# Kernel optimization log

Measured on AMD Instinct MI355X. Metric: run time of the kernel, lower is better.

The kernel has to match this reference:

```python
import jax, jax.numpy as jnp
import numpy as np

N = 100000   # nodes
E = 1600000  # edges (avg degree 16)
D = 128      # in_channels
C = 40       # out_channels (classes)
K = 3        # propagation hops


def setup_inputs() -> dict:
    key = jax.random.key(0)
    k1, k2, k3 = jax.random.split(key, 3)
    x = jax.random.normal(k1, (N, D), dtype=jnp.float32)
    edge_index = jax.random.randint(k2, (2, E), 0, N, dtype=jnp.int64)
    W = jax.random.normal(k3, (D, C), dtype=jnp.float32) * (1.0 / np.sqrt(D))
    b = jnp.zeros((C,), dtype=jnp.float32)
    return {"x": x, "edge_index": edge_index, "W": W, "b": b}


def reference(x, edge_index, W, b):
    n = x.shape[0]
    # gcn_norm: add self-loops, symmetric degree normalization
    loop = jnp.arange(n, dtype=edge_index.dtype)
    src = jnp.concatenate([edge_index[0], loop])  # [E+N]
    dst = jnp.concatenate([edge_index[1], loop])  # [E+N]
    deg = jax.ops.segment_sum(jnp.ones(src.shape[0], x.dtype), dst, num_segments=n)
    deg_inv_sqrt = jnp.where(deg > 0, jax.lax.rsqrt(deg), 0.0)
    norm = deg_inv_sqrt[src] * deg_inv_sqrt[dst]  # [E+N]
    for _ in range(K):
        x = jax.ops.segment_sum(x[src] * norm[:, None], dst, num_segments=n)
    logits = x @ W + b  # [N, C]
    return jax.nn.log_softmax(logits, axis=1)
```

## Files before the change

### kernel.cpp

```cpp
#include <hip/hip_runtime.h>

#define D 128
#define C 40
#define NBH 256
#define BSH 8
#define NBKT_MAX 512
#define EPB 6272
#define ZS 16

typedef __attribute__((ext_vector_type(8))) short s8v;
typedef __attribute__((ext_vector_type(4))) float f4v;

__device__ __forceinline__ float bf2f(unsigned short u) {
    union { unsigned int i; float f; } v; v.i = ((unsigned int)u) << 16; return v.f;
}
__device__ __forceinline__ unsigned short f2bf(float f) {
    unsigned int x = __float_as_uint(f);
    unsigned int r = (x + 0x7FFFu + ((x >> 16) & 1u)) >> 16;
    return (unsigned short)r;
}

__global__ void hist_proj_kernel(const int* __restrict__ dst, int* __restrict__ M, int E,
                                 const float* __restrict__ x, const float* __restrict__ W,
                                 unsigned short* __restrict__ y, int n, int nbkt) {
    __shared__ int shist[NBKT_MAX];
    int bid = blockIdx.x, tid = threadIdx.x;
    int role, sub;
    if (bid < 2 * NBH) { role = bid & 1; sub = bid >> 1; }
    else { role = 0; sub = bid - NBH; }

    if (role == 1) {
        for (int t = tid; t < nbkt; t += 256) shist[t] = 0;
        __syncthreads();
        int chunk = (E + NBH - 1) / NBH;
        int base = sub * chunk;
        int lim = min(E, base + chunk);
        for (int e = base + tid; e < lim; e += 256)
            atomicAdd(&shist[dst[e] >> BSH], 1);
        __syncthreads();
        for (int t = tid; t < nbkt; t += 256) M[t * NBH + sub] = shist[t];
        return;
    }

    int wid = tid >> 6;
    int lane = tid & 63;
    int tile = sub * 4 + wid;
    if (tile * 16 >= n) return;
    int r = lane & 15;
    int kg = lane >> 4;

    s8v bfrag[3][4];
#pragma unroll
    for (int ct = 0; ct < 3; ++ct) {
        int col = ct * 16 + r;
#pragma unroll
        for (int ks = 0; ks < 4; ++ks) {
            s8v f;
#pragma unroll
            for (int j = 0; j < 8; ++j) {
                int k = ks * 32 + kg * 8 + j;
                float wv = (col < C) ? W[k * C + col] : 0.0f;
                f[j] = (short)f2bf(wv);
            }
            bfrag[ct][ks] = f;
        }
    }

    f4v acc0 = {0.f, 0.f, 0.f, 0.f};
    f4v acc1 = {0.f, 0.f, 0.f, 0.f};
    f4v acc2 = {0.f, 0.f, 0.f, 0.f};
    int row = tile * 16 + r;
    const float4* xrow = (const float4*)(x + (size_t)row * D);
#pragma unroll
    for (int ks = 0; ks < 4; ++ks) {
        int kb = ks * 32 + kg * 8;
        float4 u0 = xrow[kb >> 2];
        float4 u1 = xrow[(kb >> 2) + 1];
        s8v af;
        af[0] = (short)f2bf(u0.x); af[1] = (short)f2bf(u0.y);
        af[2] = (short)f2bf(u0.z); af[3] = (short)f2bf(u0.w);
        af[4] = (short)f2bf(u1.x); af[5] = (short)f2bf(u1.y);
        af[6] = (short)f2bf(u1.z); af[7] = (short)f2bf(u1.w);
        acc0 = __builtin_amdgcn_mfma_f32_16x16x32_bf16(af, bfrag[0][ks], acc0, 0, 0, 0);
        acc1 = __builtin_amdgcn_mfma_f32_16x16x32_bf16(af, bfrag[1][ks], acc1, 0, 0, 0);
        acc2 = __builtin_amdgcn_mfma_f32_16x16x32_bf16(af, bfrag[2][ks], acc2, 0, 0, 0);
    }
#pragma unroll
    for (int rg = 0; rg < 4; ++rg) {
        int orow = tile * 16 + kg * 4 + rg;
        unsigned short* yr = y + (size_t)orow * (ZS * 4);
        yr[r] = f2bf(acc0[rg]);
        yr[16 + r] = f2bf(acc1[rg]);
        if (r < 8) yr[32 + r] = f2bf(acc2[rg]);
    }
}

__global__ void scanM_kernel(int* __restrict__ M, int* __restrict__ btot, int nbkt) {
    __shared__ int s[NBH];
    int b = blockIdx.x, tid = threadIdx.x;
    int v = M[b * NBH + tid];
    s[tid] = v;
    __syncthreads();
    for (int off = 1; off < NBH; off <<= 1) {
        int t = (tid >= off) ? s[tid - off] : 0;
        __syncthreads();
        s[tid] += t;
        __syncthreads();
    }
    M[b * NBH + tid] = s[tid] - v;
    if (tid == NBH - 1) btot[b] = s[tid];
}

__global__ void scanB_kernel(const int* __restrict__ btot, int* __restrict__ bbase,
                             int* __restrict__ rowptr, int nbkt, int n, int E) {
    __shared__ int s[512];
    int tid = threadIdx.x;
    int v = (tid < nbkt) ? btot[tid] : 0;
    s[tid] = v;
    __syncthreads();
    for (int off = 1; off < 512; off <<= 1) {
        int t = (tid >= off) ? s[tid - off] : 0;
        __syncthreads();
        s[tid] += t;
        __syncthreads();
    }
    if (tid < nbkt) bbase[tid] = s[tid] - v;
    if (tid == 0) { bbase[nbkt] = E; rowptr[n] = E; }
}

__global__ void __launch_bounds__(256)
part_kernel(const int* __restrict__ src, const int* __restrict__ dst,
            const int* __restrict__ M, const int* __restrict__ bbase,
            int* __restrict__ ebuf, int E, int nbkt) {
    __shared__ int lhist[NBKT_MAX];
    __shared__ int ls[NBKT_MAX];
    __shared__ int lslot[NBKT_MAX];
    __shared__ int sdelta[NBKT_MAX];
    __shared__ int sVal[EPB];
    __shared__ int sG[EPB];
    int blk = blockIdx.x, tid = threadIdx.x;
    int chunk = (E + NBH - 1) / NBH;
    int base = blk * chunk;
    int lim = min(E, base + chunk);
    int cnt = lim - base;

    for (int t = tid; t < NBKT_MAX; t += 256) lhist[t] = 0;
    __syncthreads();
    for (int e = base + tid; e < lim; e += 256)
        atomicAdd(&lhist[dst[e] >> BSH], 1);
    __syncthreads();
    {
        int i0 = tid, i1 = tid + 256;
        ls[i0] = lhist[i0]; ls[i1] = lhist[i1];
        __syncthreads();
        for (int off = 1; off < 512; off <<= 1) {
            int v0 = (i0 >= off) ? ls[i0 - off] : 0;
            int v1 = (i1 >= off) ? ls[i1 - off] : 0;
            __syncthreads();
            ls[i0] += v0; ls[i1] += v1;
            __syncthreads();
        }
    }
    for (int t = tid; t < nbkt; t += 256) {
        int excl = ls[t] - lhist[t];
        lslot[t] = excl;
        sdelta[t] = bbase[t] + M[t * NBH + blk] - excl;
    }
    __syncthreads();
    for (int e = base + tid; e < lim; e += 256) {
        int d = dst[e];
        int t = d >> BSH;
        int slot = atomicAdd(&lslot[t], 1);
        sVal[slot] = src[e] | ((d & ((1 << BSH) - 1)) << 17);
        sG[slot] = sdelta[t] + slot;
    }
    __syncthreads();
    for (int i = tid; i < cnt; i += 256) ebuf[sG[i]] = sVal[i];
}

__global__ void bucket_csr_kernel(const int* __restrict__ ebuf, const int* __restrict__ bbase,
                                  int* __restrict__ rowptr, float* __restrict__ dis,
                                  int* __restrict__ srcs, unsigned short* __restrict__ y, int n) {
    __shared__ int scnt[256];
    __shared__ int s[256];
    __shared__ int sptr[256];
    __shared__ float sdis[256];
    int b = blockIdx.x, tid = threadIdx.x;
    int lo = bbase[b], hi = bbase[b + 1];
    scnt[tid] = 0;
    __syncthreads();
    for (int i = lo + tid; i < hi; i += 256)
        atomicAdd(&scnt[(ebuf[i] >> 17) & 255], 1);
    __syncthreads();
    int v = scnt[tid];
    s[tid] = v;
    __syncthreads();
    for (int off = 1; off < 256; off <<= 1) {
        int t = (tid >= off) ? s[tid - off] : 0;
        __syncthreads();
        s[tid] += t;
        __syncthreads();
    }
    int excl = s[tid] - v;
    int node = b * 256 + tid;
    float dv = rsqrtf(1.0f + (float)v);
    if (node < n) { rowptr[node] = lo + excl; dis[node] = dv; }
    sdis[tid] = dv;
    sptr[tid] = lo + excl;
    __syncthreads();
    for (int i = lo + tid; i < hi; i += 256) {
        int ev = ebuf[i];
        int pos = atomicAdd(&sptr[(ev >> 17) & 255], 1);
        srcs[pos] = ev & 0x1FFFF;
    }
    __syncthreads();
    ushort4* y4 = (ushort4*)y;
    size_t base4 = (size_t)b * 256 * ZS;
    for (int idx = tid; idx < 256 * ZS; idx += 256) {
        int ch = idx & (ZS - 1);
        int node2 = b * 256 + (idx >> 4);
        if (ch < 10 && node2 < n) {
            ushort4 u = y4[base4 + idx];
            float sc = sdis[idx >> 4];
            u.x = f2bf(sc * bf2f(u.x)); u.y = f2bf(sc * bf2f(u.y));
            u.z = f2bf(sc * bf2f(u.z)); u.w = f2bf(sc * bf2f(u.w));
            y4[base4 + idx] = u;
        }
    }
}

#define ACC(vv) { ax += bf2f(vv.x); ay += bf2f(vv.y); az += bf2f(vv.z); aw += bf2f(vv.w); }

__global__ void gatherZ_kernel(const unsigned short* __restrict__ zin,
                               unsigned short* __restrict__ zout,
                               const int* __restrict__ rowptr, const int* __restrict__ srcs,
                               const float* __restrict__ dis, int n) {
    int gtid = blockIdx.x * blockDim.x + threadIdx.x;
    int node = gtid / 10;
    int ch = gtid - node * 10;
    if (node >= n) return;
    const ushort4* zi = (const ushort4*)zin;
    ushort4 sv = zi[(size_t)node * ZS + ch];
    float ax = bf2f(sv.x), ay = bf2f(sv.y), az = bf2f(sv.z), aw = bf2f(sv.w);
    int beg = rowptr[node], end = rowptr[node + 1];
    int e = beg;
    for (; e + 8 <= end; e += 8) {
        int s0 = srcs[e + 0], s1 = srcs[e + 1], s2 = srcs[e + 2], s3 = srcs[e + 3];
        int s4 = srcs[e + 4], s5 = srcs[e + 5], s6 = srcs[e + 6], s7 = srcs[e + 7];
        ushort4 v0 = zi[(size_t)s0 * ZS + ch];
        ushort4 v1 = zi[(size_t)s1 * ZS + ch];
        ushort4 v2 = zi[(size_t)s2 * ZS + ch];
        ushort4 v3 = zi[(size_t)s3 * ZS + ch];
        ushort4 v4 = zi[(size_t)s4 * ZS + ch];
        ushort4 v5 = zi[(size_t)s5 * ZS + ch];
        ushort4 v6 = zi[(size_t)s6 * ZS + ch];
        ushort4 v7 = zi[(size_t)s7 * ZS + ch];
        ACC(v0) ACC(v1) ACC(v2) ACC(v3) ACC(v4) ACC(v5) ACC(v6) ACC(v7)
    }
    for (; e + 4 <= end; e += 4) {
        int s0 = srcs[e + 0], s1 = srcs[e + 1], s2 = srcs[e + 2], s3 = srcs[e + 3];
        ushort4 v0 = zi[(size_t)s0 * ZS + ch];
        ushort4 v1 = zi[(size_t)s1 * ZS + ch];
        ushort4 v2 = zi[(size_t)s2 * ZS + ch];
        ushort4 v3 = zi[(size_t)s3 * ZS + ch];
        ACC(v0) ACC(v1) ACC(v2) ACC(v3)
    }
    for (; e < end; ++e) {
        ushort4 vv = zi[(size_t)srcs[e] * ZS + ch];
        ACC(vv)
    }
    float dd = dis[node];
    float sc = dd * dd;
    ushort4 o;
    o.x = f2bf(ax * sc); o.y = f2bf(ay * sc); o.z = f2bf(az * sc); o.w = f2bf(aw * sc);
    ((ushort4*)zout)[(size_t)node * ZS + ch] = o;
}

__global__ void __launch_bounds__(320)
gatherZ_lsm_kernel(const unsigned short* __restrict__ zin, const float* __restrict__ b,
                   float* __restrict__ out, const int* __restrict__ rowptr,
                   const int* __restrict__ srcs, const float* __restrict__ dis, int n) {
    __shared__ float sY[32 * C];
    __shared__ float sb[C];
    int tid = threadIdx.x;
    if (tid < C) sb[tid] = b[tid];
    int ndb = tid / 10;
    int ch = tid - ndb * 10;
    int node = blockIdx.x * 32 + ndb;
    if (node < n) {
        const ushort4* zi = (const ushort4*)zin;
        ushort4 sv = zi[(size_t)node * ZS + ch];
        float ax = bf2f(sv.x), ay = bf2f(sv.y), az = bf2f(sv.z), aw = bf2f(sv.w);
        int beg = rowptr[node], end = rowptr[node + 1];
        int e = beg;
        for (; e + 8 <= end; e += 8) {
            int s0 = srcs[e + 0], s1 = srcs[e + 1], s2 = srcs[e + 2], s3 = srcs[e + 3];
            int s4 = srcs[e + 4], s5 = srcs[e + 5], s6 = srcs[e + 6], s7 = srcs[e + 7];
            ushort4 v0 = zi[(size_t)s0 * ZS + ch];
            ushort4 v1 = zi[(size_t)s1 * ZS + ch];
            ushort4 v2 = zi[(size_t)s2 * ZS + ch];
            ushort4 v3 = zi[(size_t)s3 * ZS + ch];
            ushort4 v4 = zi[(size_t)s4 * ZS + ch];
            ushort4 v5 = zi[(size_t)s5 * ZS + ch];
            ushort4 v6 = zi[(size_t)s6 * ZS + ch];
            ushort4 v7 = zi[(size_t)s7 * ZS + ch];
            ACC(v0) ACC(v1) ACC(v2) ACC(v3) ACC(v4) ACC(v5) ACC(v6) ACC(v7)
        }
        for (; e + 4 <= end; e += 4) {
            int s0 = srcs[e + 0], s1 = srcs[e + 1], s2 = srcs[e + 2], s3 = srcs[e + 3];
            ushort4 v0 = zi[(size_t)s0 * ZS + ch];
            ushort4 v1 = zi[(size_t)s1 * ZS + ch];
            ushort4 v2 = zi[(size_t)s2 * ZS + ch];
            ushort4 v3 = zi[(size_t)s3 * ZS + ch];
            ACC(v0) ACC(v1) ACC(v2) ACC(v3)
        }
        for (; e < end; ++e) {
            ushort4 vv = zi[(size_t)srcs[e] * ZS + ch];
            ACC(vv)
        }
        float dd = dis[node];
        ((float4*)sY)[tid] = make_float4(ax * dd, ay * dd, az * dd, aw * dd);
    }
    __syncthreads();
    if (tid < 256) {
        int nd = tid >> 3;
        int node2 = blockIdx.x * 32 + nd;
        if (node2 < n) {
            int cg = (tid & 7) * 5;
            float a5[5];
#pragma unroll
            for (int j = 0; j < 5; ++j) a5[j] = sY[nd * C + cg + j] + sb[cg + j];
            float m = a5[0];
#pragma unroll
            for (int j = 1; j < 5; ++j) m = fmaxf(m, a5[j]);
#pragma unroll
            for (int off = 1; off < 8; off <<= 1) m = fmaxf(m, __shfl_xor(m, off, 8));
            float ssum = 0.0f;
#pragma unroll
            for (int j = 0; j < 5; ++j) ssum += __expf(a5[j] - m);
#pragma unroll
            for (int off = 1; off < 8; off <<= 1) ssum += __shfl_xor(ssum, off, 8);
            float ls = logf(ssum) + m;
            float* o = out + (size_t)node2 * C + cg;
#pragma unroll
            for (int j = 0; j < 5; ++j) o[j] = a5[j] - ls;
        }
    }
}

extern "C" void kernel_launch(void* const* d_in, const int* in_sizes, int n_in,
                              void* d_out, int out_size, void* d_ws, size_t ws_size,
                              hipStream_t stream) {
    const float* x  = (const float*)d_in[0];
    const int*   ei = (const int*)d_in[1];
    const float* W  = (const float*)d_in[2];
    const float* b  = (const float*)d_in[3];
    float* out = (float*)d_out;

    const int N = in_sizes[0] / D;
    const int E = in_sizes[1] / 2;
    const int* src = ei;
    const int* dst = ei + E;
    const int nbkt = (N + 255) >> BSH;

    size_t npad = ((size_t)N + 256) & ~(size_t)255;
    size_t epad = ((size_t)E + 255) & ~(size_t)255;
    char* p = (char*)d_ws;
    float* dis    = (float*)p;  p += npad * 4;
    int*   rowptr = (int*)p;    p += npad * 4;
    int*   btot   = (int*)p;    p += NBKT_MAX * 4;
    int*   bbase  = (int*)p;    p += (NBKT_MAX + 1) * 4;
    int*   M      = (int*)p;    p += (size_t)NBKT_MAX * NBH * 4;
    int*   ebuf   = (int*)p;    p += epad * 4;
    int*   srcs   = (int*)p;    p += epad * 4;
    size_t zpad = (((size_t)N * ZS * 8) + 255) & ~(size_t)255;
    unsigned short* zbuf0 = (unsigned short*)p;  p += zpad;
    unsigned short* zbuf1 = (unsigned short*)p;

    const int TB = 256;
    int ntile = (N + 15) / 16;
    int nb_p = (ntile + 3) / 4;

    hist_proj_kernel<<<NBH + nb_p, TB, 0, stream>>>(dst, M, E, x, W, zbuf0, N, nbkt);
    scanM_kernel<<<nbkt, NBH, 0, stream>>>(M, btot, nbkt);
    scanB_kernel<<<1, 512, 0, stream>>>(btot, bbase, rowptr, nbkt, N, E);
    part_kernel<<<NBH, TB, 0, stream>>>(src, dst, M, bbase, ebuf, E, nbkt);
    bucket_csr_kernel<<<nbkt, TB, 0, stream>>>(ebuf, bbase, rowptr, dis, srcs, zbuf0, N);

    int nb_g = ((N * 10) + TB - 1) / TB;
    gatherZ_kernel<<<nb_g, TB, 0, stream>>>(zbuf0, zbuf1, rowptr, srcs, dis, N);
    gatherZ_kernel<<<nb_g, TB, 0, stream>>>(zbuf1, zbuf0, rowptr, srcs, dis, N);
    int nb_l = (N + 31) / 32;
    gatherZ_lsm_kernel<<<nb_l, 320, 0, stream>>>(zbuf0, b, out, rowptr, srcs, dis, N);
}
```

Before: 168.9 us.

## Split projected features into two 20-channel planes for cache-resident gathers

```diff
diff --git a/kernel.cpp b/kernel.cpp
--- a/kernel.cpp
+++ b/kernel.cpp
@@ -6,7 +6,6 @@
 #define BSH 8
 #define NBKT_MAX 512
 #define EPB 6272
-#define ZS 16
 
 typedef __attribute__((ext_vector_type(8))) short s8v;
 typedef __attribute__((ext_vector_type(4))) float f4v;
@@ -22,7 +21,8 @@
 
 __global__ void hist_proj_kernel(const int* __restrict__ dst, int* __restrict__ M, int E,
                                  const float* __restrict__ x, const float* __restrict__ W,
-                                 unsigned short* __restrict__ y, int n, int nbkt) {
+                                 unsigned short* __restrict__ zlo, unsigned short* __restrict__ zhi,
+                                 int n, int nbkt) {
     __shared__ int shist[NBKT_MAX];
     int bid = blockIdx.x, tid = threadIdx.x;
     int role, sub;
@@ -88,10 +88,12 @@
 #pragma unroll
     for (int rg = 0; rg < 4; ++rg) {
         int orow = tile * 16 + kg * 4 + rg;
-        unsigned short* yr = y + (size_t)orow * (ZS * 4);
-        yr[r] = f2bf(acc0[rg]);
-        yr[16 + r] = f2bf(acc1[rg]);
-        if (r < 8) yr[32 + r] = f2bf(acc2[rg]);
+        unsigned short* lo = zlo + (size_t)orow * 20;
+        unsigned short* hi = zhi + (size_t)orow * 20;
+        lo[r] = f2bf(acc0[rg]);
+        if (r < 4) lo[16 + r] = f2bf(acc1[rg]);
+        else       hi[r - 4]  = f2bf(acc1[rg]);
+        if (r < 8) hi[12 + r] = f2bf(acc2[rg]);
     }
 }
 
@@ -180,7 +182,9 @@
 
 __global__ void bucket_csr_kernel(const int* __restrict__ ebuf, const int* __restrict__ bbase,
                                   int* __restrict__ rowptr, float* __restrict__ dis,
-                                  int* __restrict__ srcs, unsigned short* __restrict__ y, int n) {
+                                  int* __restrict__ srcs,
+                                  unsigned short* __restrict__ zlo,
+                                  unsigned short* __restrict__ zhi, int n) {
     __shared__ int scnt[256];
     __shared__ int s[256];
     __shared__ int sptr[256];
@@ -214,72 +218,77 @@
         srcs[pos] = ev & 0x1FFFF;
     }
     __syncthreads();
-    ushort4* y4 = (ushort4*)y;
-    size_t base4 = (size_t)b * 256 * ZS;
-    for (int idx = tid; idx < 256 * ZS; idx += 256) {
-        int ch = idx & (ZS - 1);
-        int node2 = b * 256 + (idx >> 4);
-        if (ch < 10 && node2 < n) {
-            ushort4 u = y4[base4 + idx];
-            float sc = sdis[idx >> 4];
+    ushort4* lo4 = (ushort4*)zlo;
+    ushort4* hi4 = (ushort4*)zhi;
+    size_t base4 = (size_t)b * 256 * 5;
+    for (int idx = tid; idx < 256 * 5; idx += 256) {
+        int node2 = b * 256 + idx / 5;
+        if (node2 < n) {
+            float sc = sdis[idx / 5];
+            ushort4 u = lo4[base4 + idx];
             u.x = f2bf(sc * bf2f(u.x)); u.y = f2bf(sc * bf2f(u.y));
             u.z = f2bf(sc * bf2f(u.z)); u.w = f2bf(sc * bf2f(u.w));
-            y4[base4 + idx] = u;
+            lo4[base4 + idx] = u;
+            ushort4 w = hi4[base4 + idx];
+            w.x = f2bf(sc * bf2f(w.x)); w.y = f2bf(sc * bf2f(w.y));
+            w.z = f2bf(sc * bf2f(w.z)); w.w = f2bf(sc * bf2f(w.w));
+            hi4[base4 + idx] = w;
         }
     }
 }
 
 #define ACC(vv) { ax += bf2f(vv.x); ay += bf2f(vv.y); az += bf2f(vv.z); aw += bf2f(vv.w); }
 
-__global__ void gatherZ_kernel(const unsigned short* __restrict__ zin,
-                               unsigned short* __restrict__ zout,
-                               const int* __restrict__ rowptr, const int* __restrict__ srcs,
-                               const float* __restrict__ dis, int n) {
-    int gtid = blockIdx.x * blockDim.x + threadIdx.x;
-    int node = gtid / 10;
-    int ch = gtid - node * 10;
+__global__ void __launch_bounds__(320)
+gatherP_kernel(const unsigned short* __restrict__ zin, unsigned short* __restrict__ zout,
+               const int* __restrict__ rowptr, const int* __restrict__ srcs,
+               const float* __restrict__ dis, int n) {
+    int tid = threadIdx.x;
+    int node = blockIdx.x * 64 + tid / 5;
+    int ch = tid - (tid / 5) * 5;
     if (node >= n) return;
     const ushort4* zi = (const ushort4*)zin;
-    ushort4 sv = zi[(size_t)node * ZS + ch];
+    ushort4 sv = zi[(size_t)node * 5 + ch];
     float ax = bf2f(sv.x), ay = bf2f(sv.y), az = bf2f(sv.z), aw = bf2f(sv.w);
     int beg = rowptr[node], end = rowptr[node + 1];
     int e = beg;
     for (; e + 8 <= end; e += 8) {
         int s0 = srcs[e + 0], s1 = srcs[e + 1], s2 = srcs[e + 2], s3 = srcs[e + 3];
         int s4 = srcs[e + 4], s5 = srcs[e + 5], s6 = srcs[e + 6], s7 = srcs[e + 7];
-        ushort4 v0 = zi[(size_t)s0 * ZS + ch];
-        ushort4 v1 = zi[(size_t)s1 * ZS + ch];
-        ushort4 v2 = zi[(size_t)s2 * ZS + ch];
-        ushort4 v3 = zi[(size_t)s3 * ZS + ch];
-        ushort4 v4 = zi[(size_t)s4 * ZS + ch];
-        ushort4 v5 = zi[(size_t)s5 * ZS + ch];
-        ushort4 v6 = zi[(size_t)s6 * ZS + ch];
-        ushort4 v7 = zi[(size_t)s7 * ZS + ch];
+        ushort4 v0 = zi[(size_t)s0 * 5 + ch];
+        ushort4 v1 = zi[(size_t)s1 * 5 + ch];
+        ushort4 v2 = zi[(size_t)s2 * 5 + ch];
+        ushort4 v3 = zi[(size_t)s3 * 5 + ch];
+        ushort4 v4 = zi[(size_t)s4 * 5 + ch];
+        ushort4 v5 = zi[(size_t)s5 * 5 + ch];
+        ushort4 v6 = zi[(size_t)s6 * 5 + ch];
+        ushort4 v7 = zi[(size_t)s7 * 5 + ch];
         ACC(v0) ACC(v1) ACC(v2) ACC(v3) ACC(v4) ACC(v5) ACC(v6) ACC(v7)
     }
     for (; e + 4 <= end; e += 4) {
         int s0 = srcs[e + 0], s1 = srcs[e + 1], s2 = srcs[e + 2], s3 = srcs[e + 3];
-        ushort4 v0 = zi[(size_t)s0 * ZS + ch];
-        ushort4 v1 = zi[(size_t)s1 * ZS + ch];
-        ushort4 v2 = zi[(size_t)s2 * ZS + ch];
-        ushort4 v3 = zi[(size_t)s3 * ZS + ch];
+        ushort4 v0 = zi[(size_t)s0 * 5 + ch];
+        ushort4 v1 = zi[(size_t)s1 * 5 + ch];
+        ushort4 v2 = zi[(size_t)s2 * 5 + ch];
+        ushort4 v3 = zi[(size_t)s3 * 5 + ch];
         ACC(v0) ACC(v1) ACC(v2) ACC(v3)
     }
     for (; e < end; ++e) {
-        ushort4 vv = zi[(size_t)srcs[e] * ZS + ch];
+        ushort4 vv = zi[(size_t)srcs[e] * 5 + ch];
         ACC(vv)
     }
     float dd = dis[node];
     float sc = dd * dd;
     ushort4 o;
     o.x = f2bf(ax * sc); o.y = f2bf(ay * sc); o.z = f2bf(az * sc); o.w = f2bf(aw * sc);
-    ((ushort4*)zout)[(size_t)node * ZS + ch] = o;
+    ((ushort4*)zout)[(size_t)node * 5 + ch] = o;
 }
 
 __global__ void __launch_bounds__(320)
-gatherZ_lsm_kernel(const unsigned short* __restrict__ zin, const float* __restrict__ b,
-                   float* __restrict__ out, const int* __restrict__ rowptr,
-                   const int* __restrict__ srcs, const float* __restrict__ dis, int n) {
+gatherZ_lsm_kernel(const unsigned short* __restrict__ zlo, const unsigned short* __restrict__ zhi,
+                   const float* __restrict__ b, float* __restrict__ out,
+                   const int* __restrict__ rowptr, const int* __restrict__ srcs,
+                   const float* __restrict__ dis, int n) {
     __shared__ float sY[32 * C];
     __shared__ float sb[C];
     int tid = threadIdx.x;
@@ -288,34 +297,35 @@
     int ch = tid - ndb * 10;
     int node = blockIdx.x * 32 + ndb;
     if (node < n) {
-        const ushort4* zi = (const ushort4*)zin;
-        ushort4 sv = zi[(size_t)node * ZS + ch];
+        const ushort4* zi = (ch < 5) ? (const ushort4*)zlo : (const ushort4*)zhi;
+        int cc = (ch < 5) ? ch : ch - 5;
+        ushort4 sv = zi[(size_t)node * 5 + cc];
         float ax = bf2f(sv.x), ay = bf2f(sv.y), az = bf2f(sv.z), aw = bf2f(sv.w);
         int beg = rowptr[node], end = rowptr[node + 1];
         int e = beg;
         for (; e + 8 <= end; e += 8) {
             int s0 = srcs[e + 0], s1 = srcs[e + 1], s2 = srcs[e + 2], s3 = srcs[e + 3];
             int s4 = srcs[e + 4], s5 = srcs[e + 5], s6 = srcs[e + 6], s7 = srcs[e + 7];
-            ushort4 v0 = zi[(size_t)s0 * ZS + ch];
-            ushort4 v1 = zi[(size_t)s1 * ZS + ch];
-            ushort4 v2 = zi[(size_t)s2 * ZS + ch];
-            ushort4 v3 = zi[(size_t)s3 * ZS + ch];
-            ushort4 v4 = zi[(size_t)s4 * ZS + ch];
-            ushort4 v5 = zi[(size_t)s5 * ZS + ch];
-            ushort4 v6 = zi[(size_t)s6 * ZS + ch];
-            ushort4 v7 = zi[(size_t)s7 * ZS + ch];
+            ushort4 v0 = zi[(size_t)s0 * 5 + cc];
+            ushort4 v1 = zi[(size_t)s1 * 5 + cc];
+            ushort4 v2 = zi[(size_t)s2 * 5 + cc];
+            ushort4 v3 = zi[(size_t)s3 * 5 + cc];
+            ushort4 v4 = zi[(size_t)s4 * 5 + cc];
+            ushort4 v5 = zi[(size_t)s5 * 5 + cc];
+            ushort4 v6 = zi[(size_t)s6 * 5 + cc];
+            ushort4 v7 = zi[(size_t)s7 * 5 + cc];
             ACC(v0) ACC(v1) ACC(v2) ACC(v3) ACC(v4) ACC(v5) ACC(v6) ACC(v7)
         }
         for (; e + 4 <= end; e += 4) {
             int s0 = srcs[e + 0], s1 = srcs[e + 1], s2 = srcs[e + 2], s3 = srcs[e + 3];
-            ushort4 v0 = zi[(size_t)s0 * ZS + ch];
-            ushort4 v1 = zi[(size_t)s1 * ZS + ch];
-            ushort4 v2 = zi[(size_t)s2 * ZS + ch];
-            ushort4 v3 = zi[(size_t)s3 * ZS + ch];
+            ushort4 v0 = zi[(size_t)s0 * 5 + cc];
+            ushort4 v1 = zi[(size_t)s1 * 5 + cc];
+            ushort4 v2 = zi[(size_t)s2 * 5 + cc];
+            ushort4 v3 = zi[(size_t)s3 * 5 + cc];
             ACC(v0) ACC(v1) ACC(v2) ACC(v3)
         }
         for (; e < end; ++e) {
-            ushort4 vv = zi[(size_t)srcs[e] * ZS + ch];
+            ushort4 vv = zi[(size_t)srcs[e] * 5 + cc];
             ACC(vv)
         }
         float dd = dis[node];
@@ -373,23 +383,28 @@
     int*   M      = (int*)p;    p += (size_t)NBKT_MAX * NBH * 4;
     int*   ebuf   = (int*)p;    p += epad * 4;
     int*   srcs   = (int*)p;    p += epad * 4;
-    size_t zpad = (((size_t)N * ZS * 8) + 255) & ~(size_t)255;
-    unsigned short* zbuf0 = (unsigned short*)p;  p += zpad;
-    unsigned short* zbuf1 = (unsigned short*)p;
+    size_t plane = (((size_t)N * 20 * 2) + 255) & ~(size_t)255;
+    unsigned short* z0lo = (unsigned short*)p;  p += plane;
+    unsigned short* z0hi = (unsigned short*)p;  p += plane;
+    unsigned short* z1lo = (unsigned short*)p;  p += plane;
+    unsigned short* z1hi = (unsigned short*)p;
 
     const int TB = 256;
     int ntile = (N + 15) / 16;
     int nb_p = (ntile + 3) / 4;
 
-    hist_proj_kernel<<<NBH + nb_p, TB, 0, stream>>>(dst, M, E, x, W, zbuf0, N, nbkt);
+    hist_proj_kernel<<<NBH + nb_p, TB, 0, stream>>>(dst, M, E, x, W, z0lo, z0hi, N, nbkt);
     scanM_kernel<<<nbkt, NBH, 0, stream>>>(M, btot, nbkt);
     scanB_kernel<<<1, 512, 0, stream>>>(btot, bbase, rowptr, nbkt, N, E);
     part_kernel<<<NBH, TB, 0, stream>>>(src, dst, M, bbase, ebuf, E, nbkt);
-    bucket_csr_kernel<<<nbkt, TB, 0, stream>>>(ebuf, bbase, rowptr, dis, srcs, zbuf0, N);
-
-    int nb_g = ((N * 10) + TB - 1) / TB;
-    gatherZ_kernel<<<nb_g, TB, 0, stream>>>(zbuf0, zbuf1, rowptr, srcs, dis, N);
-    gatherZ_kernel<<<nb_g, TB, 0, stream>>>(zbuf1, zbuf0, rowptr, srcs, dis, N);
+    bucket_csr_kernel<<<nbkt, TB, 0, stream>>>(ebuf, bbase, rowptr, dis, srcs, z0lo, z0hi, N);
+
+    int nb_g = (N + 63) / 64;
+    gatherP_kernel<<<nb_g, 320, 0, stream>>>(z0lo, z1lo, rowptr, srcs, dis, N);
+    gatherP_kernel<<<nb_g, 320, 0, stream>>>(z0hi, z1hi, rowptr, srcs, dis, N);
+    gatherP_kernel<<<nb_g, 320, 0, stream>>>(z1lo, z0lo, rowptr, srcs, dis, N);
+    gatherP_kernel<<<nb_g, 320, 0, stream>>>(z1hi, z0hi, rowptr, srcs, dis, N);
+
     int nb_l = (N + 31) / 32;
-    gatherZ_lsm_kernel<<<nb_l, 320, 0, stream>>>(zbuf0, b, out, rowptr, srcs, dis, N);
-}
+    gatherZ_lsm_kernel<<<nb_l, 320, 0, stream>>>(z0lo, z0hi, b, out, rowptr, srcs, dis, N);
+}
```

Result: slower. 201.0 us (+19.0%).
